# Performance work log

Measured on AMD Instinct MI355X. Metric: run time of the kernel, lower is better.

## Reference

```python
import jax, jax.numpy as jnp
import numpy as np

N, C, T, F = 32, 64, 256, 64  # batch, EEG channels, time samples, freq bands


def setup_inputs() -> dict:
    key = jax.random.key(0)
    X = jax.random.normal(key, (N, C, T, F), dtype=jnp.float32)
    gammad = jnp.zeros((), dtype=jnp.float32)  # learned scalar, init 'zeros'
    return {"X": X, "gammad": gammad}


def reference(X, gammad):
    # X: (N, C, T, F) -> (N, F, C, T)
    Xp = jnp.transpose(X, (0, 3, 1, 2))
    # squared norms per channel: (N, F, C, 1)
    R = jnp.sum(Xp * Xp, axis=-1, keepdims=True)
    # Gram matrix over time axis: (N, F, C, C)
    G = jnp.einsum('nfct,nfkt->nfck', Xp, Xp)
    # pairwise squared Euclidean distances between channels
    D = R - 2.0 * G + jnp.swapaxes(R, -1, -2)
    # strictly-upper-triangular entries (excludes diagonal), per (n, f)
    iu, ju = jnp.triu_indices(D.shape[-1], k=1)
    triu = jnp.sqrt(D[..., iu, ju])  # (N, F, C*(C-1)/2)
    # median bandwidth (tfp.stats.percentile q=50 uses 'nearest' interpolation)
    sigma = jnp.quantile(triu, 0.5, axis=-1, method='nearest')  # (N, F)
    denom = 2.0 * jnp.power(10.0, gammad) * jnp.square(sigma)   # (N, F)
    A = jnp.exp(-D / denom[..., None, None])  # (N, F, C, C) RBF affinity
    return A
```

## Files before the change

kernel.cpp:

```cpp
#include <hip/hip_runtime.h>
#include <stdint.h>

typedef _Float16 f16x8 __attribute__((ext_vector_type(8)));
typedef float f32x4 __attribute__((ext_vector_type(4)));

__device__ __forceinline__ uint32_t pack2(float a, float b) {
    union { _Float16 h[2]; uint32_t u; } p;
    p.h[0] = (_Float16)a; p.h[1] = (_Float16)b;
    return p.u;
}

__device__ __forceinline__ f32x4 MF(f16x8 a, f16x8 b, f32x4 c) {
    return __builtin_amdgcn_mfma_f32_16x16x32_f16(a, b, c, 0, 0, 0);
}

__device__ __forceinline__ void gram_chunk(const unsigned char* bp, f32x4 dd[2][4],
                                           int l4, int lg, int hi) {
    #pragma unroll
    for (int ks = 0; ks < 4; ++ks) {
        f16x8 fr[4];
        #pragma unroll
        for (int i2 = 0; i2 < 4; ++i2)
            fr[i2] = *(const f16x8*)(bp + (i2 * 16 + l4) * 256 +
                                     ((ks * 64 + lg * 16) ^ ((l4 & 7) << 4)));
        if (!hi) {
            #pragma unroll
            for (int tj = 0; tj < 4; ++tj) {
                dd[0][tj] = MF(fr[tj], fr[0], dd[0][tj]);
                dd[1][tj] = MF(fr[tj], fr[1], dd[1][tj]);
            }
        } else {
            #pragma unroll
            for (int tj = 0; tj < 4; ++tj) {
                dd[0][tj] = MF(fr[tj], fr[2], dd[0][tj]);
                dd[1][tj] = MF(fr[tj], fr[3], dd[1][tj]);
            }
        }
    }
}

__global__ __launch_bounds__(512, 4)
void gfc_main(const float* __restrict__ X, const float* __restrict__ gp,
              float* __restrict__ out) {
    __shared__ __align__(16) unsigned char XS[65536];
    __shared__ float Rbuf[4][64];

    int j = blockIdx.x;
    int xcd = j & 7, s = j >> 3;
    int gi = s >> 2, fq4 = s & 3;
    int g = gi * 8 + xcd;
    int n = g >> 2, f16g = g & 3;
    int f0 = f16g * 16 + fq4 * 4;

    int tid = threadIdx.x;
    int wid = tid >> 6, lane = tid & 63;
    int w4 = wid & 3, hi = wid >> 2;
    int l4 = lane & 15, lg = lane >> 4;

    float p10 = exp2f(gp[0] * 3.3219280948873623f);

    const float* Xn = X + (size_t)n * 1048576 + f0;

    f32x4 dd[2][4];
    #pragma unroll
    for (int a = 0; a < 2; ++a)
        #pragma unroll
        for (int b = 0; b < 4; ++b) dd[a][b] = f32x4{0, 0, 0, 0};

    {
        float4 v[8][2];
        #pragma unroll
        for (int k = 0; k < 8; ++k) {
            int c = k * 8 + wid;
            const float* p = Xn + (size_t)c * 16384 + lane * 128;
            v[k][0] = *(const float4*)p;
            v[k][1] = *(const float4*)(p + 64);
        }
        #pragma unroll
        for (int k = 0; k < 8; ++k) {
            int c = k * 8 + wid;
            int o = c * 256 + ((lane * 4) ^ ((c & 7) << 4));
            *(uint32_t*)(XS + o)         = pack2(v[k][0].x, v[k][1].x);
            *(uint32_t*)(XS + 16384 + o) = pack2(v[k][0].y, v[k][1].y);
            *(uint32_t*)(XS + 32768 + o) = pack2(v[k][0].z, v[k][1].z);
            *(uint32_t*)(XS + 49152 + o) = pack2(v[k][0].w, v[k][1].w);
        }
    }

    float4 pv[8][2];
    #pragma unroll
    for (int k = 0; k < 8; ++k) {
        int c = k * 8 + wid;
        const float* p = Xn + 8192 + (size_t)c * 16384 + lane * 128;
        pv[k][0] = *(const float4*)p;
        pv[k][1] = *(const float4*)(p + 64);
    }

    __syncthreads();

    gram_chunk(XS + w4 * 16384, dd, l4, lg, hi);

    __syncthreads();

    #pragma unroll
    for (int k = 0; k < 8; ++k) {
        int c = k * 8 + wid;
        int o = c * 256 + ((lane * 4) ^ ((c & 7) << 4));
        *(uint32_t*)(XS + o)         = pack2(pv[k][0].x, pv[k][1].x);
        *(uint32_t*)(XS + 16384 + o) = pack2(pv[k][0].y, pv[k][1].y);
        *(uint32_t*)(XS + 32768 + o) = pack2(pv[k][0].z, pv[k][1].z);
        *(uint32_t*)(XS + 49152 + o) = pack2(pv[k][0].w, pv[k][1].w);
    }

    __syncthreads();

    gram_chunk(XS + w4 * 16384, dd, l4, lg, hi);

    {
        f32x4 dg0 = hi ? dd[0][2] : dd[0][0];
        f32x4 dg1 = hi ? dd[1][3] : dd[1][1];
        if (lg == (l4 >> 2)) {
            int r = l4 & 3;
            float v0 = r == 0 ? dg0[0] : r == 1 ? dg0[1] : r == 2 ? dg0[2] : dg0[3];
            float v1 = r == 0 ? dg1[0] : r == 1 ? dg1[1] : r == 2 ? dg1[2] : dg1[3];
            Rbuf[w4][(hi * 2) * 16 + l4] = v0;
            Rbuf[w4][(hi * 2 + 1) * 16 + l4] = v1;
        }
    }
    __syncthreads();

    float Rr0 = Rbuf[w4][(hi * 2) * 16 + l4];
    float Rr1 = Rbuf[w4][(hi * 2 + 1) * 16 + l4];
    int keys[64];
    #pragma unroll
    for (int tj = 0; tj < 4; ++tj) {
        f32x4 Rc = *(const f32x4*)&Rbuf[w4][tj * 16 + lg * 4];
        #pragma unroll
        for (int r = 0; r < 4; ++r) {
            dd[0][tj][r] = Rr0 + Rc[r] - 2.0f * dd[0][tj][r];
            dd[1][tj][r] = Rr1 + Rc[r] - 2.0f * dd[1][tj][r];
        }
    }
    #pragma unroll
    for (int tt = 0; tt < 2; ++tt) {
        int row = (hi * 2 + tt) * 16 + l4;
        #pragma unroll
        for (int tj = 0; tj < 4; ++tj)
            #pragma unroll
            for (int r = 0; r < 4; ++r) {
                int col = tj * 16 + lg * 4 + r;
                _Float16 hx = (_Float16)fmaxf(dd[tt][tj][r], 0.0f);
                uint16_t kb = __builtin_bit_cast(uint16_t, hx);
                keys[tt * 16 + tj * 4 + r] = (row < col) ? (int)kb : 0x7FFF;
            }
    }

    {
        unsigned char* base = XS + w4 * 16384;
        uint16_t* mywr = (uint16_t*)(base + hi * 4096);
        #pragma unroll
        for (int e = 0; e < 32; ++e)
            mywr[e * 64 + lane] = (uint16_t)keys[e];
        __syncthreads();
        const uint16_t* prd = (const uint16_t*)(base + (hi ^ 1) * 4096);
        #pragma unroll
        for (int e = 0; e < 32; ++e)
            keys[32 + e] = (int)prd[e * 64 + lane];
    }

    int u = 0;
    for (int bit = 14; bit >= 0; --bit) {
        int cand = u | (1 << bit);
        int cnt = 0;
        #pragma unroll
        for (int i = 0; i < 64; ++i) cnt += (keys[i] < cand) ? 1 : 0;
        #pragma unroll
        for (int off = 32; off; off >>= 1) cnt += __shfl_xor(cnt, off, 64);
        if (cnt <= 1008) u = cand;
    }
    float sigma2 = (float)__builtin_bit_cast(_Float16, (uint16_t)u);
    float ninv = -1.0f / (2.0f * p10 * sigma2);

    float* op = out + ((size_t)(n * 64 + f0 + w4) << 12);
    #pragma unroll
    for (int tt = 0; tt < 2; ++tt) {
        int row = (hi * 2 + tt) * 16 + l4;
        #pragma unroll
        for (int tj = 0; tj < 4; ++tj) {
            float4 rv;
            rv.x = __expf(dd[tt][tj][0] * ninv);
            rv.y = __expf(dd[tt][tj][1] * ninv);
            rv.z = __expf(dd[tt][tj][2] * ninv);
            rv.w = __expf(dd[tt][tj][3] * ninv);
            *(float4*)(op + row * 64 + tj * 16 + lg * 4) = rv;
        }
    }
}

extern "C" void kernel_launch(void* const* d_in, const int* in_sizes, int n_in,
                              void* d_out, int out_size, void* d_ws, size_t ws_size,
                              hipStream_t stream) {
    (void)in_sizes; (void)n_in; (void)out_size; (void)d_ws; (void)ws_size;
    const float* X  = (const float*)d_in[0];
    const float* gp = (const float*)d_in[1];
    float* out = (float*)d_out;
    gfc_main<<<512, 512, 0, stream>>>(X, gp, out);
}
```

Measured before the change: 77.56 us.

## Double-buffer time chunks in LDS to overlap global loads with MFMA

```diff
diff --git a/kernel.cpp b/kernel.cpp
--- a/kernel.cpp
+++ b/kernel.cpp
@@ -3,6 +3,9 @@
 
 typedef _Float16 f16x8 __attribute__((ext_vector_type(8)));
 typedef float f32x4 __attribute__((ext_vector_type(4)));
+
+#define SLICE 8192
+#define BUF   32768
 
 __device__ __forceinline__ uint32_t pack2(float a, float b) {
     union { _Float16 h[2]; uint32_t u; } p;
@@ -14,35 +17,10 @@
     return __builtin_amdgcn_mfma_f32_16x16x32_f16(a, b, c, 0, 0, 0);
 }
 
-__device__ __forceinline__ void gram_chunk(const unsigned char* bp, f32x4 dd[2][4],
-                                           int l4, int lg, int hi) {
-    #pragma unroll
-    for (int ks = 0; ks < 4; ++ks) {
-        f16x8 fr[4];
-        #pragma unroll
-        for (int i2 = 0; i2 < 4; ++i2)
-            fr[i2] = *(const f16x8*)(bp + (i2 * 16 + l4) * 256 +
-                                     ((ks * 64 + lg * 16) ^ ((l4 & 7) << 4)));
-        if (!hi) {
-            #pragma unroll
-            for (int tj = 0; tj < 4; ++tj) {
-                dd[0][tj] = MF(fr[tj], fr[0], dd[0][tj]);
-                dd[1][tj] = MF(fr[tj], fr[1], dd[1][tj]);
-            }
-        } else {
-            #pragma unroll
-            for (int tj = 0; tj < 4; ++tj) {
-                dd[0][tj] = MF(fr[tj], fr[2], dd[0][tj]);
-                dd[1][tj] = MF(fr[tj], fr[3], dd[1][tj]);
-            }
-        }
-    }
-}
-
 __global__ __launch_bounds__(512, 4)
 void gfc_main(const float* __restrict__ X, const float* __restrict__ gp,
               float* __restrict__ out) {
-    __shared__ __align__(16) unsigned char XS[65536];
+    __shared__ __align__(16) unsigned char XS[2 * BUF];
     __shared__ float Rbuf[4][64];
 
     int j = blockIdx.x;
@@ -56,9 +34,9 @@
     int wid = tid >> 6, lane = tid & 63;
     int w4 = wid & 3, hi = wid >> 2;
     int l4 = lane & 15, lg = lane >> 4;
+    int tp = lane & 31, cs = lane >> 5;
 
     float p10 = exp2f(gp[0] * 3.3219280948873623f);
-
     const float* Xn = X + (size_t)n * 1048576 + f0;
 
     f32x4 dd[2][4];
@@ -67,54 +45,77 @@
         #pragma unroll
         for (int b = 0; b < 4; ++b) dd[a][b] = f32x4{0, 0, 0, 0};
 
-    {
-        float4 v[8][2];
-        #pragma unroll
-        for (int k = 0; k < 8; ++k) {
-            int c = k * 8 + wid;
-            const float* p = Xn + (size_t)c * 16384 + lane * 128;
-            v[k][0] = *(const float4*)p;
-            v[k][1] = *(const float4*)(p + 64);
-        }
-        #pragma unroll
-        for (int k = 0; k < 8; ++k) {
-            int c = k * 8 + wid;
-            int o = c * 256 + ((lane * 4) ^ ((c & 7) << 4));
-            *(uint32_t*)(XS + o)         = pack2(v[k][0].x, v[k][1].x);
-            *(uint32_t*)(XS + 16384 + o) = pack2(v[k][0].y, v[k][1].y);
-            *(uint32_t*)(XS + 32768 + o) = pack2(v[k][0].z, v[k][1].z);
-            *(uint32_t*)(XS + 49152 + o) = pack2(v[k][0].w, v[k][1].w);
-        }
-    }
-
-    float4 pv[8][2];
-    #pragma unroll
-    for (int k = 0; k < 8; ++k) {
-        int c = k * 8 + wid;
-        const float* p = Xn + 8192 + (size_t)c * 16384 + lane * 128;
-        pv[k][0] = *(const float4*)p;
-        pv[k][1] = *(const float4*)(p + 64);
-    }
-
-    __syncthreads();
-
-    gram_chunk(XS + w4 * 16384, dd, l4, lg, hi);
-
-    __syncthreads();
-
-    #pragma unroll
-    for (int k = 0; k < 8; ++k) {
-        int c = k * 8 + wid;
-        int o = c * 256 + ((lane * 4) ^ ((c & 7) << 4));
-        *(uint32_t*)(XS + o)         = pack2(pv[k][0].x, pv[k][1].x);
-        *(uint32_t*)(XS + 16384 + o) = pack2(pv[k][0].y, pv[k][1].y);
-        *(uint32_t*)(XS + 32768 + o) = pack2(pv[k][0].z, pv[k][1].z);
-        *(uint32_t*)(XS + 49152 + o) = pack2(pv[k][0].w, pv[k][1].w);
-    }
-
-    __syncthreads();
-
-    gram_chunk(XS + w4 * 16384, dd, l4, lg, hi);
+    float4 pv[4][2];
+
+    auto load_chunk = [&](int t0) {
+        #pragma unroll
+        for (int b = 0; b < 4; ++b) {
+            int c = wid * 8 + b * 2 + cs;
+            const float* p = Xn + ((size_t)c * 256 + t0 + 2 * tp) * 64;
+            pv[b][0] = *(const float4*)p;
+            pv[b][1] = *(const float4*)(p + 64);
+        }
+    };
+    auto write_chunk = [&](unsigned char* B) {
+        #pragma unroll
+        for (int b = 0; b < 4; ++b) {
+            int c = wid * 8 + b * 2 + cs;
+            int o = c * 128 + ((tp * 4) ^ ((c & 7) << 4));
+            *(uint32_t*)(B + 0 * SLICE + o) = pack2(pv[b][0].x, pv[b][1].x);
+            *(uint32_t*)(B + 1 * SLICE + o) = pack2(pv[b][0].y, pv[b][1].y);
+            *(uint32_t*)(B + 2 * SLICE + o) = pack2(pv[b][0].z, pv[b][1].z);
+            *(uint32_t*)(B + 3 * SLICE + o) = pack2(pv[b][0].w, pv[b][1].w);
+        }
+    };
+    auto gram_buf = [&](const unsigned char* bp) {
+        #pragma unroll
+        for (int ks = 0; ks < 2; ++ks) {
+            f16x8 fr[4];
+            #pragma unroll
+            for (int i2 = 0; i2 < 4; ++i2)
+                fr[i2] = *(const f16x8*)(bp + (i2 * 16 + l4) * 128 +
+                                         ((ks * 64 + lg * 16) ^ ((l4 & 7) << 4)));
+            if (!hi) {
+                #pragma unroll
+                for (int tj = 0; tj < 4; ++tj) {
+                    dd[0][tj] = MF(fr[tj], fr[0], dd[0][tj]);
+                    dd[1][tj] = MF(fr[tj], fr[1], dd[1][tj]);
+                }
+            } else {
+                #pragma unroll
+                for (int tj = 0; tj < 4; ++tj) {
+                    dd[0][tj] = MF(fr[tj], fr[2], dd[0][tj]);
+                    dd[1][tj] = MF(fr[tj], fr[3], dd[1][tj]);
+                }
+            }
+        }
+    };
+
+    unsigned char* buf0 = XS;
+    unsigned char* buf1 = XS + BUF;
+    const unsigned char* g0 = buf0 + w4 * SLICE;
+    const unsigned char* g1 = buf1 + w4 * SLICE;
+
+    load_chunk(0);
+    write_chunk(buf0);
+    load_chunk(64);
+    __syncthreads();
+
+    gram_buf(g0);
+    write_chunk(buf1);
+    load_chunk(128);
+    __syncthreads();
+
+    gram_buf(g1);
+    write_chunk(buf0);
+    load_chunk(192);
+    __syncthreads();
+
+    gram_buf(g0);
+    write_chunk(buf1);
+    __syncthreads();
+
+    gram_buf(g1);
 
     {
         f32x4 dg0 = hi ? dd[0][2] : dd[0][0];
```

After: 69.34 us. 10.6% less time.
